# Kernel optimization log

Measured on AMD Instinct MI355X. Metric: run time of the kernel, lower is better.

The kernel has to match this reference:

```python
import jax, jax.numpy as jnp
import numpy as np

B, N, L = 8, 170, 336
PATCH = 16
P = L // PATCH            # 21 patches, pad_len = 0
D_MODEL = 128
D_STATE = 16
D_CONV = 4
D_INNER = 2 * D_MODEL     # expand=2
DT_RANK = 8               # ceil(d_model/16)
PRED_LEN = 96


def setup_inputs() -> dict:
    key = jax.random.key(0)
    ks = jax.random.split(key, 16)
    def nrm(k, shape, s=0.02):
        return jax.random.normal(k, shape, jnp.float32) * s
    return {
        "x": jax.random.normal(ks[0], (B, N, L), jnp.float32),
        "node_embed_map": nrm(ks[1], (1, N, 1, D_MODEL)),
        "pe_W": nrm(ks[2], (D_MODEL, PATCH), 0.1),
        "pe_b": jnp.zeros((D_MODEL,), jnp.float32),
        "pos_emb": nrm(ks[3], (1, 1, P, D_MODEL)),
        "r_W1": nrm(ks[4], (D_MODEL // 4, 3), 0.3),
        "r_b1": jnp.zeros((D_MODEL // 4,), jnp.float32),
        "r_W2": nrm(ks[5], (D_MODEL, D_MODEL // 4), 0.1),
        "r_b2": jnp.zeros((D_MODEL,), jnp.float32),
        "ln_g": jnp.ones((D_MODEL,), jnp.float32),
        "ln_b": jnp.zeros((D_MODEL,), jnp.float32),
        "in_proj_W": nrm(ks[6], (2 * D_INNER, D_MODEL), 0.05),
        "conv_W": nrm(ks[7], (D_INNER, D_CONV), 0.2),
        "conv_b": jnp.zeros((D_INNER,), jnp.float32),
        "x_proj_W": nrm(ks[8], (DT_RANK + 2 * D_STATE, D_INNER), 0.05),
        "dt_proj_W": nrm(ks[9], (D_INNER, DT_RANK), 0.3),
        "dt_proj_b": nrm(ks[10], (D_INNER,), 0.5),
        "A_log": jnp.log(jnp.broadcast_to(jnp.arange(1.0, D_STATE + 1.0, dtype=jnp.float32), (D_INNER, D_STATE))),
        "D_skip": jnp.ones((D_INNER,), jnp.float32),
        "out_proj_W": nrm(ks[11], (D_MODEL, D_INNER), 0.05),
        "head_W": nrm(ks[12], (PRED_LEN, P * D_MODEL), 0.02),
        "head_b": jnp.zeros((PRED_LEN,), jnp.float32),
    }


def _layernorm(x, g, b, eps=1e-5):
    mu = x.mean(-1, keepdims=True)
    var = ((x - mu) ** 2).mean(-1, keepdims=True)
    return (x - mu) * jax.lax.rsqrt(var + eps) * g + b


def _router(x_patch, r_W1, r_b1, r_W2, r_b2):
    # FFT energy over each length-16 patch -> low/mid/high band features -> tiny MLP gate
    X = jnp.fft.rfft(x_patch, axis=-1)          # [M, P, 9]
    energy = X.real ** 2 + X.imag ** 2
    fl = energy.shape[-1]
    s1, s2 = fl // 3, 2 * fl // 3
    feats = jnp.stack([energy[..., :s1].sum(-1),
                       energy[..., s1:s2].sum(-1),
                       energy[..., s2:].sum(-1)], axis=-1)
    feats = feats / (feats.sum(-1, keepdims=True) + 1e-6)
    h = jax.nn.relu(feats @ r_W1.T + r_b1)
    return jax.nn.sigmoid(h @ r_W2.T + r_b2)    # [M, P, d_model]


def _mamba(u, in_proj_W, conv_W, conv_b, x_proj_W, dt_proj_W, dt_proj_b, A_log, D_skip, out_proj_W):
    # u: [M, T, d_model]  (Mamba block: in_proj -> causal dwconv -> SSM scan -> gate -> out_proj)
    M, T, _ = u.shape
    xz = u @ in_proj_W.T                        # [M, T, 2*d_inner]
    xc, z = jnp.split(xz, 2, axis=-1)
    # causal depthwise conv1d, kernel D_CONV
    xp = jnp.pad(xc, ((0, 0), (D_CONV - 1, 0), (0, 0)))
    conv = conv_b + sum(xp[:, k:k + T, :] * conv_W[:, k] for k in range(D_CONV))
    xs = jax.nn.silu(conv)                      # [M, T, d_inner]
    proj = xs @ x_proj_W.T                      # [M, T, dt_rank + 2*d_state]
    dt_in = proj[..., :DT_RANK]
    Bm = proj[..., DT_RANK:DT_RANK + D_STATE]
    Cm = proj[..., DT_RANK + D_STATE:]
    dt = jax.nn.softplus(dt_in @ dt_proj_W.T + dt_proj_b)  # [M, T, d_inner]
    A = -jnp.exp(A_log)                         # [d_inner, d_state]

    def step(h, inp):
        dt_t, B_t, C_t, u_t = inp               # [M,d_inner], [M,d_state], [M,d_state], [M,d_inner]
        dA = jnp.exp(dt_t[..., None] * A)       # [M, d_inner, d_state]
        h = dA * h + (dt_t * u_t)[..., None] * B_t[:, None, :]
        y = jnp.einsum('mds,ms->md', h, C_t)
        return h, y

    h0 = jnp.zeros((M, D_INNER, D_STATE), jnp.float32)
    _, ys = jax.lax.scan(step, h0, (jnp.moveaxis(dt, 1, 0), jnp.moveaxis(Bm, 1, 0),
                                    jnp.moveaxis(Cm, 1, 0), jnp.moveaxis(xs, 1, 0)))
    y = jnp.moveaxis(ys, 0, 1) + xs * D_skip
    y = y * jax.nn.silu(z)
    return y @ out_proj_W.T


def reference(x, node_embed_map, pe_W, pe_b, pos_emb, r_W1, r_b1, r_W2, r_b2,
              ln_g, ln_b, in_proj_W, conv_W, conv_b, x_proj_W, dt_proj_W, dt_proj_b,
              A_log, D_skip, out_proj_W, head_W, head_b):
    Bb, Nn, _ = x.shape
    x_patches = x.reshape(Bb, Nn, P, PATCH)                     # pad_len == 0 for L=336
    x_enc = x_patches @ pe_W.T + pe_b + pos_emb + node_embed_map
    x_enc_flat = x_enc.reshape(Bb * Nn, P, D_MODEL)
    gate = _router(x_patches.reshape(Bb * Nn, P, PATCH), r_W1, r_b1, r_W2, r_b2)
    x_gated = _layernorm(x_enc_flat, ln_g, ln_b) * gate
    y = _mamba(x_gated, in_proj_W, conv_W, conv_b, x_proj_W, dt_proj_W, dt_proj_b,
               A_log, D_skip, out_proj_W)
    out = (y + x_enc_flat).reshape(Bb, Nn, P * D_MODEL)         # dropout is identity (eval)
    return out @ head_W.T + head_b                              # [B, N, pred_len]
```

## Files before the change

### kernel.cpp

```cpp
#include <hip/hip_runtime.h>
#include <math.h>

#define B_ 8
#define N_ 170
#define L_ 336
#define PATCH_ 16
#define P_ 21
#define DM_ 128
#define DS_ 16
#define DI_ 256
#define PL_ 96
#define M_ (B_ * N_)
#define T_ 21
#define R_ (M_ * T_)
#define KF_ (P_ * DM_)
#define UST 136
#define XROW 264

typedef __attribute__((ext_vector_type(8))) short short8;
typedef __attribute__((ext_vector_type(4))) float f32x4;

__device__ inline unsigned short f2b(float f) {
    unsigned int u = __builtin_bit_cast(unsigned int, f);
    u += 0x7fff + ((u >> 16) & 1);
    return (unsigned short)(u >> 16);
}
__device__ inline float b2f(unsigned short h) {
    unsigned int u = ((unsigned int)h) << 16;
    return __builtin_bit_cast(float, u);
}
__device__ inline float fast_sigmoid(float v) {
    return __builtin_amdgcn_rcpf(1.f + __expf(-v));
}

__global__ __launch_bounds__(256) void k_convert(
    const float* __restrict__ inW, const float* __restrict__ xpW,
    const float* __restrict__ outW, const float* __restrict__ hW,
    unsigned short* __restrict__ winb, unsigned short* __restrict__ wxpb,
    unsigned short* __restrict__ woutb, unsigned short* __restrict__ whb)
{
    int i = blockIdx.x * 256 + threadIdx.x;
    if (i < 65536) { winb[i] = f2b(inW[i]); return; }
    i -= 65536;
    if (i < 16384) {
        int j = i >> 8;
        wxpb[i] = (j < 40) ? f2b(xpW[j * 256 + (i & 255)]) : (unsigned short)0;
        return;
    }
    i -= 16384;
    if (i < 32768) { woutb[i] = f2b(outW[i]); return; }
    i -= 32768;
    if (i < 258048) { whb[i] = f2b(hW[i]); }
}

__global__ __launch_bounds__(256) void k_fused(
    const float* __restrict__ x, const float* __restrict__ nem,
    const float* __restrict__ peW, const float* __restrict__ peB,
    const float* __restrict__ posE,
    const float* __restrict__ rW1, const float* __restrict__ rB1,
    const float* __restrict__ rW2, const float* __restrict__ rB2,
    const float* __restrict__ lnG, const float* __restrict__ lnB,
    const unsigned short* __restrict__ winb,
    const float* __restrict__ convW, const float* __restrict__ convB,
    const unsigned short* __restrict__ wxpb,
    const float* __restrict__ dtW, const float* __restrict__ dtB,
    const float* __restrict__ Dsk,
    const unsigned short* __restrict__ woutb,
    unsigned short* __restrict__ feat)
{
    __shared__ unsigned short us[32 * UST];
    __shared__ unsigned short xencs[T_ * 132];
    __shared__ __align__(16) char scratch[31360];

    const int m = blockIdx.x;
    const int n = m % N_;
    const int tid = threadIdx.x;
    const int lane = tid & 63;
    const int w = tid >> 6;

    {
        float* sf   = (float*)scratch;
        float* xls  = sf;
        float* ct   = sf + 336;
        float* st   = sf + 352;
        float* peWs = sf + 368;
        float* rws  = sf + 2544;
        float* es   = sf + 6768;
        float* hs   = sf + 6957;

        const float peB0 = peB[lane],           peB1 = peB[lane + 64];
        const float nem0 = nem[n * DM_ + lane], nem1 = nem[n * DM_ + lane + 64];
        const float lg0 = lnG[lane], lg1 = lnG[lane + 64];
        const float lb0 = lnB[lane], lb1 = lnB[lane + 64];
        const float rb0 = rB2[lane], rb1 = rB2[lane + 64];

        for (int i = tid; i < L_; i += 256) xls[i] = x[m * L_ + i];
        for (int i = tid; i < DM_ * PATCH_; i += 256)
            peWs[(i >> 4) * 17 + (i & 15)] = peW[i];
        for (int i = tid; i < DM_ * 32; i += 256)
            rws[(i >> 5) * 33 + (i & 31)] = rW2[i];
        if (tid < 16) {
            float s, c;
            sincosf((float)tid * (6.283185307179586f / 16.f), &s, &c);
            ct[tid] = c; st[tid] = s;
        }
        {
            int* usI = (int*)us;
            for (int i = tid; i < 11 * (UST / 2); i += 256)
                usI[21 * (UST / 2) + i] = 0;
        }
        __syncthreads();

        for (int i = tid; i < P_ * 9; i += 256) {
            const int p = i / 9, bin = i - p * 9;
            const float* xp = &xls[p * PATCH_];
            float re = 0.f, im = 0.f;
#pragma unroll
            for (int j = 0; j < PATCH_; ++j) {
                int idx = (bin * j) & 15;
                re = fmaf(xp[j], ct[idx], re);
                im = fmaf(xp[j], -st[idx], im);
            }
            es[i] = re * re + im * im;
        }
        __syncthreads();

        for (int idx = tid; idx < P_ * 32; idx += 256) {
            const int p = idx >> 5, i = idx & 31;
            const float* e = &es[p * 9];
            float b0 = e[0] + e[1] + e[2];
            float b1 = e[3] + e[4] + e[5];
            float b2 = e[6] + e[7] + e[8];
            float inv = __builtin_amdgcn_rcpf(b0 + b1 + b2 + 1e-6f);
            float hv = rB1[i];
            hv = fmaf(b0 * inv, rW1[i * 3 + 0], hv);
            hv = fmaf(b1 * inv, rW1[i * 3 + 1], hv);
            hv = fmaf(b2 * inv, rW1[i * 3 + 2], hv);
            hs[idx] = hv > 0.f ? hv : 0.f;
        }
        __syncthreads();

        for (int it = 0; it < 6; ++it) {
            const int p = it * 4 + w;
            if (p >= P_) continue;

            float xe0 = peB0 + posE[p * DM_ + lane] + nem0;
            float xe1 = peB1 + posE[p * DM_ + lane + 64] + nem1;
            const float* xp = &xls[p * PATCH_];
            const float* pw0 = &peWs[lane * 17];
            const float* pw1 = &peWs[(lane + 64) * 17];
#pragma unroll
            for (int j = 0; j < PATCH_; ++j) {
                float xv = xp[j];
                xe0 = fmaf(pw0[j], xv, xe0);
                xe1 = fmaf(pw1[j], xv, xe1);
            }

            const float* hp = &hs[p * 32];
            const float* rw0 = &rws[lane * 33];
            const float* rw1 = &rws[(lane + 64) * 33];
            float g0 = rb0, g1 = rb1;
#pragma unroll
            for (int i = 0; i < 32; ++i) {
                float hv = hp[i];
                g0 = fmaf(rw0[i], hv, g0);
                g1 = fmaf(rw1[i], hv, g1);
            }
            g0 = fast_sigmoid(g0);
            g1 = fast_sigmoid(g1);

            float s = xe0 + xe1, s2 = xe0 * xe0 + xe1 * xe1;
#pragma unroll
            for (int off = 32; off; off >>= 1) {
                s += __shfl_xor(s, off);
                s2 += __shfl_xor(s2, off);
            }
            float mu = s * (1.f / 128.f);
            float var = s2 * (1.f / 128.f) - mu * mu;
            float rs = rsqrtf(var + 1e-5f);
            float u0 = ((xe0 - mu) * rs * lg0 + lb0) * g0;
            float u1 = ((xe1 - mu) * rs * lg1 + lb1) * g1;

            us[p * UST + lane]      = f2b(u0);
            us[p * UST + 64 + lane] = f2b(u1);
            xencs[p * 132 + lane]      = f2b(xe0);
            xencs[p * 132 + 64 + lane] = f2b(xe1);
        }
    }
    __syncthreads();

    unsigned short* xss = (unsigned short*)scratch;
    unsigned short* zls = xss + 32 * XROW;
    float* pjs = (float*)(scratch + (32 + 21) * XROW * 2);

    {
        int* xsI = (int*)xss;
        for (int i = tid; i < 11 * (XROW / 2); i += 256)
            xsI[21 * (XROW / 2) + i] = 0;

        const int lo = lane & 15, kq = (lane >> 4) * 8;
        f32x4 C[2][8];
#pragma unroll
        for (int mi = 0; mi < 2; ++mi)
#pragma unroll
            for (int ni = 0; ni < 8; ++ni) C[mi][ni] = (f32x4){0.f, 0.f, 0.f, 0.f};

        const unsigned short* bbase = winb + (size_t)(w * 128 + lo) * DM_ + kq;
#pragma unroll
        for (int k0 = 0; k0 < DM_; k0 += 32) {
            short8 a0 = *(const short8*)&us[lo * UST + k0 + kq];
            short8 a1 = *(const short8*)&us[(16 + lo) * UST + k0 + kq];
#pragma unroll
            for (int ni = 0; ni < 8; ++ni) {
                short8 b = *(const short8*)(bbase + ni * 16 * DM_ + k0);
                C[0][ni] = __builtin_amdgcn_mfma_f32_16x16x32_bf16(a0, b, C[0][ni], 0, 0, 0);
                C[1][ni] = __builtin_amdgcn_mfma_f32_16x16x32_bf16(a1, b, C[1][ni], 0, 0, 0);
            }
        }
        const int rl = (lane >> 4) * 4, cl = lane & 15;
        unsigned short* dst = (w < 2) ? xss : zls;
        const int cbase = (w & 1) * 128 + cl;
#pragma unroll
        for (int ni = 0; ni < 8; ++ni) {
            const int col = cbase + ni * 16;
#pragma unroll
            for (int mi = 0; mi < 2; ++mi)
#pragma unroll
                for (int r = 0; r < 4; ++r) {
                    const int row = mi * 16 + rl + r;
                    if (row < T_) dst[row * XROW + col] = f2b(C[mi][ni][r]);
                }
        }
    }
    __syncthreads();

    {
        const int d = tid;
        float4 cw = *(const float4*)(convW + d * 4);
        const float cb = convB[d];
        float c0 = 0.f, c1 = 0.f, c2 = 0.f;
#pragma unroll
        for (int t = 0; t < T_; ++t) {
            float c3 = b2f(xss[t * XROW + d]);
            float v = cb;
            v = fmaf(c0, cw.x, v);
            v = fmaf(c1, cw.y, v);
            v = fmaf(c2, cw.z, v);
            v = fmaf(c3, cw.w, v);
            v = v * fast_sigmoid(v);
            xss[t * XROW + d] = f2b(v);
            c0 = c1; c1 = c2; c2 = c3;
        }
    }
    __syncthreads();

    {
        const int mt = w >> 1, nt = w & 1;
        const int lo = lane & 15, kq = (lane >> 4) * 8;
        const unsigned short* ar = &xss[(mt * 16 + lo) * XROW + kq];
        const unsigned short* bp0 = wxpb + (nt * 32 + lo) * DI_ + kq;
        const unsigned short* bp1 = bp0 + 16 * DI_;
        f32x4 c0 = {0.f, 0.f, 0.f, 0.f}, c1 = c0;
#pragma unroll
        for (int k0 = 0; k0 < DI_; k0 += 32) {
            short8 a  = *(const short8*)(ar + k0);
            short8 b0 = *(const short8*)(bp0 + k0);
            short8 b1 = *(const short8*)(bp1 + k0);
            c0 = __builtin_amdgcn_mfma_f32_16x16x32_bf16(a, b0, c0, 0, 0, 0);
            c1 = __builtin_amdgcn_mfma_f32_16x16x32_bf16(a, b1, c1, 0, 0, 0);
        }
        const int rl = (lane >> 4) * 4, cl = lane & 15;
#pragma unroll
        for (int r = 0; r < 4; ++r) {
            const int row = mt * 16 + rl + r;
            const int ca = nt * 32 + cl, cb = ca + 16;
            if (row < T_) {
                if (ca < 40) pjs[row * 40 + ca] = c0[r];
                if (cb < 40) pjs[row * 40 + cb] = c1[r];
            }
        }
    }
    __syncthreads();

    {
        const int d = tid;
        float dw[8];
        *(float4*)&dw[0] = *(const float4*)(dtW + d * 8);
        *(float4*)&dw[4] = *(const float4*)(dtW + d * 8 + 4);
        const float db = dtB[d], Dv = Dsk[d];
        const f32x4* pj4 = (const f32x4*)pjs;
        float h[DS_];
#pragma unroll
        for (int s = 0; s < DS_; ++s) h[s] = 0.f;
#pragma unroll
        for (int t = 0; t < T_; ++t) {
            f32x4 d0 = pj4[t * 10 + 0], d1 = pj4[t * 10 + 1];
            f32x4 Bv[4], Cv[4];
#pragma unroll
            for (int q = 0; q < 4; ++q) { Bv[q] = pj4[t * 10 + 2 + q]; Cv[q] = pj4[t * 10 + 6 + q]; }
            float a = db;
#pragma unroll
            for (int r = 0; r < 4; ++r) a = fmaf(d0[r], dw[r], a);
#pragma unroll
            for (int r = 0; r < 4; ++r) a = fmaf(d1[r], dw[4 + r], a);
            float dt = (a > 20.f) ? a : __logf(1.f + __expf(a));
            float ut = b2f(xss[t * XROW + d]);
            float zv = b2f(zls[t * XROW + d]);
            float wk = dt * ut;
            float e1 = __expf(-dt);
            float dA = 1.f;
            float yv = 0.f;
#pragma unroll
            for (int s = 0; s < DS_; ++s) {
                dA *= e1;
                h[s] = fmaf(dA, h[s], wk * Bv[s >> 2][s & 3]);
                yv = fmaf(h[s], Cv[s >> 2][s & 3], yv);
            }
            yv = fmaf(ut, Dv, yv);
            yv *= zv * fast_sigmoid(zv);
            xss[t * XROW + d] = f2b(yv);
        }
    }
    __syncthreads();

    {
        const int lo = lane & 15, kq = (lane >> 4) * 8;
        f32x4 C[2][2];
#pragma unroll
        for (int mi = 0; mi < 2; ++mi)
#pragma unroll
            for (int ni = 0; ni < 2; ++ni) C[mi][ni] = (f32x4){0.f, 0.f, 0.f, 0.f};

        const unsigned short* bbase = woutb + (size_t)(w * 32 + lo) * DI_ + kq;
#pragma unroll
        for (int k0 = 0; k0 < DI_; k0 += 32) {
            short8 a0 = *(const short8*)&xss[lo * XROW + k0 + kq];
            short8 a1 = *(const short8*)&xss[(16 + lo) * XROW + k0 + kq];
#pragma unroll
            for (int ni = 0; ni < 2; ++ni) {
                short8 b = *(const short8*)(bbase + ni * 16 * DI_ + k0);
                C[0][ni] = __builtin_amdgcn_mfma_f32_16x16x32_bf16(a0, b, C[0][ni], 0, 0, 0);
                C[1][ni] = __builtin_amdgcn_mfma_f32_16x16x32_bf16(a1, b, C[1][ni], 0, 0, 0);
            }
        }
        const int rl = (lane >> 4) * 4, cl = lane & 15;
        unsigned short* fb = feat + (size_t)m * T_ * DM_;
#pragma unroll
        for (int mi = 0; mi < 2; ++mi)
#pragma unroll
            for (int r = 0; r < 4; ++r) {
                const int row = mi * 16 + rl + r;
                if (row < T_) {
#pragma unroll
                    for (int ni = 0; ni < 2; ++ni) {
                        const int col = w * 32 + ni * 16 + cl;
                        float res = b2f(xencs[row * 132 + col]);
                        fb[row * DM_ + col] = f2b(C[mi][ni][r] + res);
                    }
                }
            }
    }
}

__global__ __launch_bounds__(256) void k_gemm_head(
    const unsigned short* __restrict__ feat, const unsigned short* __restrict__ W,
    const float* __restrict__ hB, float* __restrict__ out)
{
    __shared__ float red[4 * 512];
    const int bid = blockIdx.x;
    const int wm = bid / 3, wn = bid % 3;
    const int tid = threadIdx.x, w = tid >> 6, lane = tid & 63;
    const int r0 = wm * 16, n0 = wn * 32;
    const int lo = lane & 15, kq = (lane >> 4) * 8;
    const int kb = w * 672;
    const unsigned short* ap  = feat + (size_t)(r0 + lo) * KF_ + kb + kq;
    const unsigned short* bp0 = W + (size_t)(n0 + lo) * KF_ + kb + kq;
    const unsigned short* bp1 = bp0 + 16 * KF_;
    f32x4 c0 = {0.f, 0.f, 0.f, 0.f}, c1 = c0;
#pragma unroll 3
    for (int k0 = 0; k0 < 672; k0 += 32) {
        short8 a  = *(const short8*)(ap + k0);
        short8 b0 = *(const short8*)(bp0 + k0);
        short8 b1 = *(const short8*)(bp1 + k0);
        c0 = __builtin_amdgcn_mfma_f32_16x16x32_bf16(a, b0, c0, 0, 0, 0);
        c1 = __builtin_amdgcn_mfma_f32_16x16x32_bf16(a, b1, c1, 0, 0, 0);
    }
    float* rw = &red[w * 512 + lane * 8];
#pragma unroll
    for (int r = 0; r < 4; ++r) { rw[r] = c0[r]; rw[4 + r] = c1[r]; }
    __syncthreads();

    for (int f = tid; f < 512; f += 256) {
        float s = red[f] + red[512 + f] + red[1024 + f] + red[1536 + f];
        const int l = f >> 3, v = f & 7;
        const int row = r0 + ((l >> 4) << 2) + (v & 3);
        const int col = n0 + (l & 15) + ((v >= 4) ? 16 : 0);
        out[row * PL_ + col] = s + hB[col];
    }
}

extern "C" void kernel_launch(void* const* d_in, const int* in_sizes, int n_in,
                              void* d_out, int out_size, void* d_ws, size_t ws_size,
                              hipStream_t stream)
{
    const float* x     = (const float*)d_in[0];
    const float* nem   = (const float*)d_in[1];
    const float* peW   = (const float*)d_in[2];
    const float* peB   = (const float*)d_in[3];
    const float* posE  = (const float*)d_in[4];
    const float* rW1   = (const float*)d_in[5];
    const float* rB1   = (const float*)d_in[6];
    const float* rW2   = (const float*)d_in[7];
    const float* rB2   = (const float*)d_in[8];
    const float* lnG   = (const float*)d_in[9];
    const float* lnB   = (const float*)d_in[10];
    const float* inW   = (const float*)d_in[11];
    const float* convW = (const float*)d_in[12];
    const float* convB = (const float*)d_in[13];
    const float* xpW   = (const float*)d_in[14];
    const float* dtW   = (const float*)d_in[15];
    const float* dtB   = (const float*)d_in[16];
    const float* Dsk   = (const float*)d_in[18];
    const float* outW  = (const float*)d_in[19];
    const float* hW    = (const float*)d_in[20];
    const float* hB    = (const float*)d_in[21];
    float* out = (float*)d_out;

    char* ws = (char*)d_ws;
    size_t off = 0;
    auto alloc = [&](size_t bytes) { size_t o = off; off = (off + bytes + 255) & ~(size_t)255; return o; };
    unsigned short* feat  = (unsigned short*)(ws + alloc((size_t)R_ * DM_ * 2));
    unsigned short* winb  = (unsigned short*)(ws + alloc(512 * 128 * 2));
    unsigned short* wxpb  = (unsigned short*)(ws + alloc(64 * 256 * 2));
    unsigned short* woutb = (unsigned short*)(ws + alloc(128 * 256 * 2));
    unsigned short* whb   = (unsigned short*)(ws + alloc(96 * KF_ * 2));

    k_convert<<<1456, 256, 0, stream>>>(inW, xpW, outW, hW, winb, wxpb, woutb, whb);
    k_fused<<<M_, 256, 0, stream>>>(x, nem, peW, peB, posE,
                                    rW1, rB1, rW2, rB2, lnG, lnB,
                                    winb, convW, convB, wxpb,
                                    dtW, dtB, Dsk, woutb, feat);
    k_gemm_head<<<255, 256, 0, stream>>>(feat, whb, hB, out);
}
```

Before: 216.1 us.

## Move patch embedding and router MLP onto MFMA and compact LDS layout

Converts peW and rW2 to bf16 in the convert kernel and computes the patch embedding and router second layer with bf16 MFMA instead of scalar FMA loops. It overlays LDS buffers to shrink shared memory and adds launch bounds targeting 4 blocks per SM for higher occupancy. It also precomputes silu(z) when storing the in-projection output and derives exp(-dt) from the softplus exponential with a reciprocal. The change adds bf16 rounding to the embedding, posE and gate values and introduces an extra barrier.

After: 192.3 us. 11.0% less time.

```diff
diff --git a/kernel.cpp b/kernel.cpp
--- a/kernel.cpp
+++ b/kernel.cpp
@@ -14,8 +14,6 @@
 #define T_ 21
 #define R_ (M_ * T_)
 #define KF_ (P_ * DM_)
-#define UST 136
-#define XROW 264
 
 typedef __attribute__((ext_vector_type(8))) short short8;
 typedef __attribute__((ext_vector_type(4))) float f32x4;
@@ -36,8 +34,10 @@
 __global__ __launch_bounds__(256) void k_convert(
     const float* __restrict__ inW, const float* __restrict__ xpW,
     const float* __restrict__ outW, const float* __restrict__ hW,
+    const float* __restrict__ peW, const float* __restrict__ rW2,
     unsigned short* __restrict__ winb, unsigned short* __restrict__ wxpb,
-    unsigned short* __restrict__ woutb, unsigned short* __restrict__ whb)
+    unsigned short* __restrict__ woutb, unsigned short* __restrict__ whb,
+    unsigned short* __restrict__ peWb, unsigned short* __restrict__ rW2b)
 {
     int i = blockIdx.x * 256 + threadIdx.x;
     if (i < 65536) { winb[i] = f2b(inW[i]); return; }
@@ -50,15 +50,23 @@
     i -= 16384;
     if (i < 32768) { woutb[i] = f2b(outW[i]); return; }
     i -= 32768;
-    if (i < 258048) { whb[i] = f2b(hW[i]); }
-}
-
-__global__ __launch_bounds__(256) void k_fused(
+    if (i < 258048) { whb[i] = f2b(hW[i]); return; }
+    i -= 258048;
+    if (i < 4096) {
+        int r = i >> 5, j = i & 31;
+        peWb[i] = (j < 16) ? f2b(peW[r * 16 + j]) : (unsigned short)0;
+        return;
+    }
+    i -= 4096;
+    if (i < 4096) { rW2b[i] = f2b(rW2[i]); }
+}
+
+__global__ __launch_bounds__(256, 4) void k_fused(
     const float* __restrict__ x, const float* __restrict__ nem,
-    const float* __restrict__ peW, const float* __restrict__ peB,
+    const unsigned short* __restrict__ peWb, const float* __restrict__ peB,
     const float* __restrict__ posE,
     const float* __restrict__ rW1, const float* __restrict__ rB1,
-    const float* __restrict__ rW2, const float* __restrict__ rB2,
+    const unsigned short* __restrict__ rW2b, const float* __restrict__ rB2,
     const float* __restrict__ lnG, const float* __restrict__ lnB,
     const unsigned short* __restrict__ winb,
     const float* __restrict__ convW, const float* __restrict__ convB,
@@ -68,107 +76,144 @@
     const unsigned short* __restrict__ woutb,
     unsigned short* __restrict__ feat)
 {
-    __shared__ unsigned short us[32 * UST];
-    __shared__ unsigned short xencs[T_ * 132];
-    __shared__ __align__(16) char scratch[31360];
+    __shared__ __align__(16) char lds[36896];
+    unsigned short* xencs = (unsigned short*)(lds + 0);
+    unsigned short* us    = (unsigned short*)(lds + 5552);
+    unsigned short* zsl   = (unsigned short*)(lds + 5552);
+    unsigned short* xss   = (unsigned short*)(lds + 16640);
+    float*          pjs   = (float*)(lds + 33536);
+    float*          xls   = (float*)(lds + 14256);
+    float*          ctst  = (float*)(lds + 15600);
+    unsigned short* pa    = (unsigned short*)(lds + 15728);
+    unsigned short* ha    = (unsigned short*)(lds + 18288);
+    float*          es    = (float*)(lds + 20848);
+    unsigned short* gs    = (unsigned short*)(lds + 21608);
+    float*          pn    = (float*)(lds + 27160);
+    unsigned short* posEs = (unsigned short*)(lds + 27672);
 
     const int m = blockIdx.x;
     const int n = m % N_;
     const int tid = threadIdx.x;
     const int lane = tid & 63;
     const int w = tid >> 6;
-
-    {
-        float* sf   = (float*)scratch;
-        float* xls  = sf;
-        float* ct   = sf + 336;
-        float* st   = sf + 352;
-        float* peWs = sf + 368;
-        float* rws  = sf + 2544;
-        float* es   = sf + 6768;
-        float* hs   = sf + 6957;
-
-        const float peB0 = peB[lane],           peB1 = peB[lane + 64];
-        const float nem0 = nem[n * DM_ + lane], nem1 = nem[n * DM_ + lane + 64];
+    const int lo = lane & 15, kq = (lane >> 4) * 8;
+    const int rl = (lane >> 4) * 4, cl = lane & 15;
+
+    for (int i = tid; i < L_; i += 256) xls[i] = x[m * L_ + i];
+    for (int i = tid; i < 32 * 40; i += 256) {
+        const int p = i / 40, j = i - p * 40;
+        pa[i] = (p < P_ && j < PATCH_) ? f2b(x[m * L_ + p * PATCH_ + j])
+                                       : (unsigned short)0;
+        ha[i] = 0;
+    }
+    if (tid < 16) {
+        float s, c;
+        sincosf((float)tid * (6.283185307179586f / 16.f), &s, &c);
+        ctst[tid] = c; ctst[16 + tid] = s;
+    }
+    if (tid >= 64 && tid < 192) pn[tid - 64] = peB[tid - 64] + nem[n * DM_ + tid - 64];
+    for (int i = tid; i < P_ * DM_; i += 256)
+        posEs[(i >> 7) * 132 + (i & 127)] = f2b(posE[i]);
+    {
+        int* usI = (int*)us;
+        for (int i = tid; i < 11 * 68; i += 256) usI[21 * 68 + i] = 0;
+    }
+    __syncthreads();
+
+    for (int i = tid; i < P_ * 9; i += 256) {
+        const int p = i / 9, bin = i - p * 9;
+        const float* xp = &xls[p * PATCH_];
+        float re = 0.f, im = 0.f;
+#pragma unroll
+        for (int j = 0; j < PATCH_; ++j) {
+            int idx = (bin * j) & 15;
+            re = fmaf(xp[j], ctst[idx], re);
+            im = fmaf(xp[j], -ctst[16 + idx], im);
+        }
+        es[i] = re * re + im * im;
+    }
+    __syncthreads();
+
+    for (int idx = tid; idx < P_ * 32; idx += 256) {
+        const int p = idx >> 5, i = idx & 31;
+        const float* e = &es[p * 9];
+        float b0 = e[0] + e[1] + e[2];
+        float b1 = e[3] + e[4] + e[5];
+        float b2 = e[6] + e[7] + e[8];
+        float inv = __builtin_amdgcn_rcpf(b0 + b1 + b2 + 1e-6f);
+        float hv = rB1[i];
+        hv = fmaf(b0 * inv, rW1[i * 3 + 0], hv);
+        hv = fmaf(b1 * inv, rW1[i * 3 + 1], hv);
+        hv = fmaf(b2 * inv, rW1[i * 3 + 2], hv);
+        ha[p * 40 + i] = f2b(hv > 0.f ? hv : 0.f);
+    }
+    {
+        const unsigned short* bb = peWb + (w * 32 + lo) * 32 + kq;
+        short8 b0 = *(const short8*)bb;
+        short8 b1 = *(const short8*)(bb + 16 * 32);
+        short8 a0 = *(const short8*)&pa[lo * 40 + kq];
+        short8 a1 = *(const short8*)&pa[(16 + lo) * 40 + kq];
+        f32x4 z = {0.f, 0.f, 0.f, 0.f};
+        f32x4 C[2][2];
+        C[0][0] = __builtin_amdgcn_mfma_f32_16x16x32_bf16(a0, b0, z, 0, 0, 0);
+        C[0][1] = __builtin_amdgcn_mfma_f32_16x16x32_bf16(a0, b1, z, 0, 0, 0);
+        C[1][0] = __builtin_amdgcn_mfma_f32_16x16x32_bf16(a1, b0, z, 0, 0, 0);
+        C[1][1] = __builtin_amdgcn_mfma_f32_16x16x32_bf16(a1, b1, z, 0, 0, 0);
+#pragma unroll
+        for (int mi = 0; mi < 2; ++mi)
+#pragma unroll
+            for (int r = 0; r < 4; ++r) {
+                const int row = mi * 16 + rl + r;
+                if (row < P_) {
+#pragma unroll
+                    for (int ni = 0; ni < 2; ++ni) {
+                        const int col = w * 32 + ni * 16 + cl;
+                        float xe = C[mi][ni][r] + pn[col] + b2f(posEs[row * 132 + col]);
+                        xencs[row * 132 + col] = f2b(xe);
+                    }
+                }
+            }
+    }
+    __syncthreads();
+
+    {
+        const unsigned short* bb = rW2b + (w * 32 + lo) * 32 + kq;
+        short8 b0 = *(const short8*)bb;
+        short8 b1 = *(const short8*)(bb + 16 * 32);
+        short8 a0 = *(const short8*)&ha[lo * 40 + kq];
+        short8 a1 = *(const short8*)&ha[(16 + lo) * 40 + kq];
+        f32x4 z = {0.f, 0.f, 0.f, 0.f};
+        f32x4 C[2][2];
+        C[0][0] = __builtin_amdgcn_mfma_f32_16x16x32_bf16(a0, b0, z, 0, 0, 0);
+        C[0][1] = __builtin_amdgcn_mfma_f32_16x16x32_bf16(a0, b1, z, 0, 0, 0);
+        C[1][0] = __builtin_amdgcn_mfma_f32_16x16x32_bf16(a1, b0, z, 0, 0, 0);
+        C[1][1] = __builtin_amdgcn_mfma_f32_16x16x32_bf16(a1, b1, z, 0, 0, 0);
+#pragma unroll
+        for (int mi = 0; mi < 2; ++mi)
+#pragma unroll
+            for (int r = 0; r < 4; ++r) {
+                const int row = mi * 16 + rl + r;
+                if (row < P_) {
+#pragma unroll
+                    for (int ni = 0; ni < 2; ++ni) {
+                        const int col = w * 32 + ni * 16 + cl;
+                        gs[row * 132 + col] = f2b(fast_sigmoid(C[mi][ni][r] + rB2[col]));
+                    }
+                }
+            }
+    }
+    __syncthreads();
+
+    {
         const float lg0 = lnG[lane], lg1 = lnG[lane + 64];
         const float lb0 = lnB[lane], lb1 = lnB[lane + 64];
-        const float rb0 = rB2[lane], rb1 = rB2[lane + 64];
-
-        for (int i = tid; i < L_; i += 256) xls[i] = x[m * L_ + i];
-        for (int i = tid; i < DM_ * PATCH_; i += 256)
-            peWs[(i >> 4) * 17 + (i & 15)] = peW[i];
-        for (int i = tid; i < DM_ * 32; i += 256)
-            rws[(i >> 5) * 33 + (i & 31)] = rW2[i];
-        if (tid < 16) {
-            float s, c;
-            sincosf((float)tid * (6.283185307179586f / 16.f), &s, &c);
-            ct[tid] = c; st[tid] = s;
-        }
-        {
-            int* usI = (int*)us;
-            for (int i = tid; i < 11 * (UST / 2); i += 256)
-                usI[21 * (UST / 2) + i] = 0;
-        }
-        __syncthreads();
-
-        for (int i = tid; i < P_ * 9; i += 256) {
-            const int p = i / 9, bin = i - p * 9;
-            const float* xp = &xls[p * PATCH_];
-            float re = 0.f, im = 0.f;
-#pragma unroll
-            for (int j = 0; j < PATCH_; ++j) {
-                int idx = (bin * j) & 15;
-                re = fmaf(xp[j], ct[idx], re);
-                im = fmaf(xp[j], -st[idx], im);
-            }
-            es[i] = re * re + im * im;
-        }
-        __syncthreads();
-
-        for (int idx = tid; idx < P_ * 32; idx += 256) {
-            const int p = idx >> 5, i = idx & 31;
-            const float* e = &es[p * 9];
-            float b0 = e[0] + e[1] + e[2];
-            float b1 = e[3] + e[4] + e[5];
-            float b2 = e[6] + e[7] + e[8];
-            float inv = __builtin_amdgcn_rcpf(b0 + b1 + b2 + 1e-6f);
-            float hv = rB1[i];
-            hv = fmaf(b0 * inv, rW1[i * 3 + 0], hv);
-            hv = fmaf(b1 * inv, rW1[i * 3 + 1], hv);
-            hv = fmaf(b2 * inv, rW1[i * 3 + 2], hv);
-            hs[idx] = hv > 0.f ? hv : 0.f;
-        }
-        __syncthreads();
-
         for (int it = 0; it < 6; ++it) {
             const int p = it * 4 + w;
             if (p >= P_) continue;
-
-            float xe0 = peB0 + posE[p * DM_ + lane] + nem0;
-            float xe1 = peB1 + posE[p * DM_ + lane + 64] + nem1;
-            const float* xp = &xls[p * PATCH_];
-            const float* pw0 = &peWs[lane * 17];
-            const float* pw1 = &peWs[(lane + 64) * 17];
-#pragma unroll
-            for (int j = 0; j < PATCH_; ++j) {
-                float xv = xp[j];
-                xe0 = fmaf(pw0[j], xv, xe0);
-                xe1 = fmaf(pw1[j], xv, xe1);
-            }
-
-            const float* hp = &hs[p * 32];
-            const float* rw0 = &rws[lane * 33];
-            const float* rw1 = &rws[(lane + 64) * 33];
-            float g0 = rb0, g1 = rb1;
-#pragma unroll
-            for (int i = 0; i < 32; ++i) {
-                float hv = hp[i];
-                g0 = fmaf(rw0[i], hv, g0);
-                g1 = fmaf(rw1[i], hv, g1);
-            }
-            g0 = fast_sigmoid(g0);
-            g1 = fast_sigmoid(g1);
-
+            float xe0 = b2f(xencs[p * 132 + lane]);
+            float xe1 = b2f(xencs[p * 132 + 64 + lane]);
+            float g0 = b2f(gs[p * 132 + lane]);
+            float g1 = b2f(gs[p * 132 + 64 + lane]);
             float s = xe0 + xe1, s2 = xe0 * xe0 + xe1 * xe1;
 #pragma unroll
             for (int off = 32; off; off >>= 1) {
@@ -178,27 +223,13 @@
             float mu = s * (1.f / 128.f);
             float var = s2 * (1.f / 128.f) - mu * mu;
             float rs = rsqrtf(var + 1e-5f);
-            float u0 = ((xe0 - mu) * rs * lg0 + lb0) * g0;
-            float u1 = ((xe1 - mu) * rs * lg1 + lb1) * g1;
-
-            us[p * UST + lane]      = f2b(u0);
-            us[p * UST + 64 + lane] = f2b(u1);
-            xencs[p * 132 + lane]      = f2b(xe0);
-            xencs[p * 132 + 64 + lane] = f2b(xe1);
-        }
-    }
-    __syncthreads();
-
-    unsigned short* xss = (unsigned short*)scratch;
-    unsigned short* zls = xss + 32 * XROW;
-    float* pjs = (float*)(scratch + (32 + 21) * XROW * 2);
-
-    {
-        int* xsI = (int*)xss;
-        for (int i = tid; i < 11 * (XROW / 2); i += 256)
-            xsI[21 * (XROW / 2) + i] = 0;
-
-        const int lo = lane & 15, kq = (lane >> 4) * 8;
+            us[p * 136 + lane]      = f2b(((xe0 - mu) * rs * lg0 + lb0) * g0);
+            us[p * 136 + 64 + lane] = f2b(((xe1 - mu) * rs * lg1 + lb1) * g1);
+        }
+    }
+    __syncthreads();
+
+    {
         f32x4 C[2][8];
 #pragma unroll
         for (int mi = 0; mi < 2; ++mi)
@@ -208,8 +239,8 @@
         const unsigned short* bbase = winb + (size_t)(w * 128 + lo) * DM_ + kq;
 #pragma unroll
         for (int k0 = 0; k0 < DM_; k0 += 32) {
-            short8 a0 = *(const short8*)&us[lo * UST + k0 + kq];
-            short8 a1 = *(const short8*)&us[(16 + lo) * UST + k0 + kq];
+            short8 a0 = *(const short8*)&us[lo * 136 + k0 + kq];
+            short8 a1 = *(const short8*)&us[(16 + lo) * 136 + k0 + kq];
 #pragma unroll
             for (int ni = 0; ni < 8; ++ni) {
                 short8 b = *(const short8*)(bbase + ni * 16 * DM_ + k0);
@@ -217,19 +248,40 @@
                 C[1][ni] = __builtin_amdgcn_mfma_f32_16x16x32_bf16(a1, b, C[1][ni], 0, 0, 0);
             }
         }
-        const int rl = (lane >> 4) * 4, cl = lane & 15;
-        unsigned short* dst = (w < 2) ? xss : zls;
+        __syncthreads();
+
+        {
+            int* xsI = (int*)xss;
+            for (int i = tid; i < 11 * 132; i += 256) xsI[21 * 132 + i] = 0;
+        }
         const int cbase = (w & 1) * 128 + cl;
-#pragma unroll
-        for (int ni = 0; ni < 8; ++ni) {
-            const int col = cbase + ni * 16;
-#pragma unroll
-            for (int mi = 0; mi < 2; ++mi)
-#pragma unroll
-                for (int r = 0; r < 4; ++r) {
-                    const int row = mi * 16 + rl + r;
-                    if (row < T_) dst[row * XROW + col] = f2b(C[mi][ni][r]);
-                }
+        if (w < 2) {
+#pragma unroll
+            for (int ni = 0; ni < 8; ++ni) {
+                const int col = cbase + ni * 16;
+#pragma unroll
+                for (int mi = 0; mi < 2; ++mi)
+#pragma unroll
+                    for (int r = 0; r < 4; ++r) {
+                        const int row = mi * 16 + rl + r;
+                        if (row < T_) xss[row * 264 + col] = f2b(C[mi][ni][r]);
+                    }
+            }
+        } else {
+#pragma unroll
+            for (int ni = 0; ni < 8; ++ni) {
+                const int col = cbase + ni * 16;
+#pragma unroll
+                for (int mi = 0; mi < 2; ++mi)
+#pragma unroll
+                    for (int r = 0; r < 4; ++r) {
+                        const int row = mi * 16 + rl + r;
+                        if (row < T_) {
+                            float v = C[mi][ni][r];
+                            zsl[row * 264 + col] = f2b(v * fast_sigmoid(v));
+                        }
+                    }
+            }
         }
     }
     __syncthreads();
@@ -241,14 +293,14 @@
         float c0 = 0.f, c1 = 0.f, c2 = 0.f;
 #pragma unroll
         for (int t = 0; t < T_; ++t) {
-            float c3 = b2f(xss[t * XROW + d]);
+            float c3 = b2f(xss[t * 264 + d]);
             float v = cb;
             v = fmaf(c0, cw.x, v);
             v = fmaf(c1, cw.y, v);
             v = fmaf(c2, cw.z, v);
             v = fmaf(c3, cw.w, v);
             v = v * fast_sigmoid(v);
-            xss[t * XROW + d] = f2b(v);
+            xss[t * 264 + d] = f2b(v);
             c0 = c1; c1 = c2; c2 = c3;
         }
     }
@@ -256,8 +308,7 @@
 
     {
         const int mt = w >> 1, nt = w & 1;
-        const int lo = lane & 15, kq = (lane >> 4) * 8;
-        const unsigned short* ar = &xss[(mt * 16 + lo) * XROW + kq];
+        const unsigned short* ar = &xss[(mt * 16 + lo) * 264 + kq];
         const unsigned short* bp0 = wxpb + (nt * 32 + lo) * DI_ + kq;
         const unsigned short* bp1 = bp0 + 16 * DI_;
         f32x4 c0 = {0.f, 0.f, 0.f, 0.f}, c1 = c0;
@@ -269,7 +320,6 @@
             c0 = __builtin_amdgcn_mfma_f32_16x16x32_bf16(a, b0, c0, 0, 0, 0);
             c1 = __builtin_amdgcn_mfma_f32_16x16x32_bf16(a, b1, c1, 0, 0, 0);
         }
-        const int rl = (lane >> 4) * 4, cl = lane & 15;
 #pragma unroll
         for (int r = 0; r < 4; ++r) {
             const int row = mt * 16 + rl + r;
@@ -303,11 +353,12 @@
             for (int r = 0; r < 4; ++r) a = fmaf(d0[r], dw[r], a);
 #pragma unroll
             for (int r = 0; r < 4; ++r) a = fmaf(d1[r], dw[4 + r], a);
-            float dt = (a > 20.f) ? a : __logf(1.f + __expf(a));
-            float ut = b2f(xss[t * XROW + d]);
-            float zv = b2f(zls[t * XROW + d]);
+            float qe = __expf(a);
+            float dt = (a > 20.f) ? a : __logf(1.f + qe);
+            float e1 = __builtin_amdgcn_rcpf(1.f + qe);
+            float ut = b2f(xss[t * 264 + d]);
+            float zq = b2f(zsl[t * 264 + d]);
             float wk = dt * ut;
-            float e1 = __expf(-dt);
             float dA = 1.f;
             float yv = 0.f;
 #pragma unroll
@@ -316,15 +367,13 @@
                 h[s] = fmaf(dA, h[s], wk * Bv[s >> 2][s & 3]);
                 yv = fmaf(h[s], Cv[s >> 2][s & 3], yv);
             }
-            yv = fmaf(ut, Dv, yv);
-            yv *= zv * fast_sigmoid(zv);
-            xss[t * XROW + d] = f2b(yv);
-        }
-    }
-    __syncthreads();
-
-    {
-        const int lo = lane & 15, kq = (lane >> 4) * 8;
+            yv = fmaf(ut, Dv, yv) * zq;
+            xss[t * 264 + d] = f2b(yv);
+        }
+    }
+    __syncthreads();
+
+    {
         f32x4 C[2][2];
 #pragma unroll
         for (int mi = 0; mi < 2; ++mi)
@@ -334,8 +383,8 @@
         const unsigned short* bbase = woutb + (size_t)(w * 32 + lo) * DI_ + kq;
 #pragma unroll
         for (int k0 = 0; k0 < DI_; k0 += 32) {
-            short8 a0 = *(const short8*)&xss[lo * XROW + k0 + kq];
-            short8 a1 = *(const short8*)&xss[(16 + lo) * XROW + k0 + kq];
+            short8 a0 = *(const short8*)&xss[lo * 264 + k0 + kq];
+            short8 a1 = *(const short8*)&xss[(16 + lo) * 264 + k0 + kq];
 #pragma unroll
             for (int ni = 0; ni < 2; ++ni) {
                 short8 b = *(const short8*)(bbase + ni * 16 * DI_ + k0);
@@ -343,7 +392,6 @@
                 C[1][ni] = __builtin_amdgcn_mfma_f32_16x16x32_bf16(a1, b, C[1][ni], 0, 0, 0);
             }
         }
-        const int rl = (lane >> 4) * 4, cl = lane & 15;
         unsigned short* fb = feat + (size_t)m * T_ * DM_;
 #pragma unroll
         for (int mi = 0; mi < 2; ++mi)
@@ -434,10 +482,13 @@
     unsigned short* wxpb  = (unsigned short*)(ws + alloc(64 * 256 * 2));
     unsigned short* woutb = (unsigned short*)(ws + alloc(128 * 256 * 2));
     unsigned short* whb   = (unsigned short*)(ws + alloc(96 * KF_ * 2));
-
-    k_convert<<<1456, 256, 0, stream>>>(inW, xpW, outW, hW, winb, wxpb, woutb, whb);
-    k_fused<<<M_, 256, 0, stream>>>(x, nem, peW, peB, posE,
-                                    rW1, rB1, rW2, rB2, lnG, lnB,
+    unsigned short* peWb  = (unsigned short*)(ws + alloc(128 * 32 * 2));
+    unsigned short* rW2b  = (unsigned short*)(ws + alloc(128 * 32 * 2));
+
+    k_convert<<<1488, 256, 0, stream>>>(inW, xpW, outW, hW, peW, rW2,
+                                        winb, wxpb, woutb, whb, peWb, rW2b);
+    k_fused<<<M_, 256, 0, stream>>>(x, nem, peWb, peB, posE,
+                                    rW1, rB1, rW2b, rB2, lnG, lnB,
                                     winb, convW, convB, wxpb,
                                     dtW, dtB, Dsk, woutb, feat);
     k_gemm_head<<<255, 256, 0, stream>>>(feat, whb, hB, out);
```
